# Performance work log

Measured on AMD Instinct MI355X. Metric: run time of the kernel, lower is better.

Reference implementation:

```python
import jax, jax.numpy as jnp
import numpy as np

H_DIM = 256
N_HEADS = 8
HEAD_DIM = H_DIM // N_HEADS
B, N = 2, 2048
LN_EPS = 1e-5


def setup_inputs() -> dict:
    key = jax.random.key(0)
    ks = jax.random.split(key, 20)
    s = 1.0 / np.sqrt(H_DIM)
    inp = {
        'hidden': jax.random.normal(ks[0], (B, N, H_DIM), jnp.float32),
        'adjacency': jax.random.uniform(ks[1], (B, N, N), jnp.float32),
        'positions': jax.random.uniform(ks[2], (B, N, 2), jnp.float32),
        # linear weights stored as (in, out): y = x @ W + b
        'wq': jax.random.normal(ks[3], (H_DIM, H_DIM), jnp.float32) * s,
        'bq': jnp.zeros((H_DIM,), jnp.float32),
        'wk': jax.random.normal(ks[4], (H_DIM, H_DIM), jnp.float32) * s,
        'bk': jnp.zeros((H_DIM,), jnp.float32),
        'wv': jax.random.normal(ks[5], (H_DIM, H_DIM), jnp.float32) * s,
        'bv': jnp.zeros((H_DIM,), jnp.float32),
        'wo': jax.random.normal(ks[6], (H_DIM, H_DIM), jnp.float32) * s,
        'bo': jnp.zeros((H_DIM,), jnp.float32),
        'g1': jnp.ones((H_DIM,), jnp.float32),
        'b1': jnp.zeros((H_DIM,), jnp.float32),
        'g2': jnp.ones((H_DIM,), jnp.float32),
        'b2': jnp.zeros((H_DIM,), jnp.float32),
        'w_ff1': jax.random.normal(ks[7], (H_DIM, 4 * H_DIM), jnp.float32) * s,
        'b_ff1': jnp.zeros((4 * H_DIM,), jnp.float32),
        'w_ff2': jax.random.normal(ks[8], (4 * H_DIM, H_DIM), jnp.float32) * (1.0 / np.sqrt(4 * H_DIM)),
        'b_ff2': jnp.zeros((H_DIM,), jnp.float32),
    }
    return inp


def _layernorm(x, g, b):
    mu = jnp.mean(x, axis=-1, keepdims=True)
    var = jnp.var(x, axis=-1, keepdims=True)
    return (x - mu) * jax.lax.rsqrt(var + LN_EPS) * g + b


def reference(hidden, adjacency, positions, wq, bq, wk, bk, wv, bv, wo, bo,
              g1, b1, g2, b2, w_ff1, b_ff1, w_ff2, b_ff2):
    b_, n_, _ = hidden.shape
    normalized = _layernorm(hidden, g1, b1)
    # project and split heads: [B, H, N, Dh]
    def heads(x):
        return x.reshape(b_, n_, N_HEADS, HEAD_DIM).transpose(0, 2, 1, 3)
    q = heads(normalized @ wq + bq)
    k = heads(normalized @ wk + bk)
    v = heads(normalized @ wv + bv)
    logits = jnp.einsum('bhnd,bhmd->bhnm', q, k) / np.sqrt(HEAD_DIM)
    cond = adjacency[:, None, :, :]  # mode == 'connectivity'
    logits = logits + (2.0 * cond - 1.0)
    weights = jax.nn.softmax(logits, axis=-1)
    weights = weights * (0.25 + 0.75 * cond)
    weights = weights / jnp.maximum(weights.sum(axis=-1, keepdims=True), 1e-6)
    attended = jnp.einsum('bhnm,bhmd->bhnd', weights, v)
    attended = attended.transpose(0, 2, 1, 3).reshape(b_, n_, H_DIM)
    hidden = hidden + attended @ wo + bo
    h2 = _layernorm(hidden, g2, b2)
    ff = jax.nn.gelu(h2 @ w_ff1 + b_ff1, approximate=False) @ w_ff2 + b_ff2
    return hidden + ff
```

## Files before the change

kernel.cpp:

```cpp
#include <hip/hip_runtime.h>
#include <math.h>

#define BB 2
#define NN 2048
#define HD 256
#define NH 8
#define DH 32
#define NTOK (BB*NN)
#define QKVLD 768
#define NSPLIT 2
#define KVPB (NN/NSPLIT)
#define NTILES (KVPB/64)

typedef _Float16 h8 __attribute__((ext_vector_type(8)));
typedef _Float16 h4 __attribute__((ext_vector_type(4)));
typedef float fx4 __attribute__((ext_vector_type(4)));

#define LOG2E 1.4426950408889634f
#define SQ_LOG2 0.25503486f
#define C1A (2.0f * LOG2E)
#define C0A (-(LOG2E + 6.0f))

__device__ __forceinline__ void ln_row(const float* __restrict__ x,
    const float* __restrict__ g, const float* __restrict__ bta,
    _Float16* __restrict__ yh, int row, int lane)
{
  const float* xr = x + (size_t)row * HD + lane * 4;
  float4 v = *(const float4*)xr;
  float s = v.x + v.y + v.z + v.w;
  #pragma unroll
  for (int off = 32; off > 0; off >>= 1) s += __shfl_xor(s, off);
  float mu = s * (1.0f / HD);
  float dx0 = v.x - mu, dx1 = v.y - mu, dx2 = v.z - mu, dx3 = v.w - mu;
  float ss = dx0*dx0 + dx1*dx1 + dx2*dx2 + dx3*dx3;
  #pragma unroll
  for (int off = 32; off > 0; off >>= 1) ss += __shfl_xor(ss, off);
  float rinv = rsqrtf(ss * (1.0f / HD) + 1e-5f);
  float4 gv = *(const float4*)(g   + lane * 4);
  float4 bv = *(const float4*)(bta + lane * 4);
  h4 hh;
  hh[0] = (_Float16)(dx0 * rinv * gv.x + bv.x);
  hh[1] = (_Float16)(dx1 * rinv * gv.y + bv.y);
  hh[2] = (_Float16)(dx2 * rinv * gv.z + bv.z);
  hh[3] = (_Float16)(dx3 * rinv * gv.w + bv.w);
  *(h4*)(yh + (size_t)row * HD + lane * 4) = hh;
}

__global__ __launch_bounds__(256) void ln_kernel(const float* __restrict__ x,
    const float* __restrict__ g, const float* __restrict__ bta,
    _Float16* __restrict__ yh)
{
  ln_row(x, g, bta, yh, blockIdx.x * 4 + (threadIdx.x >> 6), threadIdx.x & 63);
}

__device__ __forceinline__ void do_transpose(const float* __restrict__ W,
    _Float16* __restrict__ Wh, int Nw, int rowoff, int ldout, float scale,
    int bx, int by, float (*tile)[33])
{
  int k0 = by * 32, n0 = bx * 32;
  int c = threadIdx.x & 31, r = threadIdx.x >> 5;
  #pragma unroll
  for (int i = 0; i < 4; i++)
    tile[r + i * 8][c] = W[(size_t)(k0 + r + i * 8) * Nw + n0 + c];
  __syncthreads();
  #pragma unroll
  for (int i = 0; i < 4; i++) {
    int n = r + i * 8;
    Wh[(size_t)(rowoff + n0 + n) * ldout + k0 + c] = (_Float16)(tile[c][n] * scale);
  }
}

__global__ __launch_bounds__(256) void prep_kernel(
    const float* wq, const float* wk, const float* wv, const float* wo,
    const float* wf1, const float* wf2,
    const float* bq, const float* bk, const float* bv,
    const float* hidden, const float* g1, const float* b1,
    _Float16* WtQKVh, _Float16* WtOh, _Float16* WtF1h, _Float16* WtF2h,
    float* biasqkv, _Float16* norm1h)
{
  __shared__ float tile[32][33];
  int bid = blockIdx.x;
  if (bid < 64)        do_transpose(wq,  WtQKVh,  256,   0,  256, SQ_LOG2, bid & 7, bid >> 3, tile);
  else if (bid < 128)  do_transpose(wk,  WtQKVh,  256, 256,  256, 1.0f, (bid-64) & 7, (bid-64) >> 3, tile);
  else if (bid < 192)  do_transpose(wv,  WtQKVh,  256, 512,  256, 1.0f, (bid-128) & 7, (bid-128) >> 3, tile);
  else if (bid < 256)  do_transpose(wo,  WtOh,    256,   0,  256, 1.0f, (bid-192) & 7, (bid-192) >> 3, tile);
  else if (bid < 512)  do_transpose(wf1, WtF1h,  1024,   0,  256, 1.0f, (bid-256) & 31, (bid-256) >> 5, tile);
  else if (bid < 768)  do_transpose(wf2, WtF2h,   256,   0, 1024, 1.0f, (bid-512) & 7, (bid-512) >> 3, tile);
  else if (bid == 768) {
    #pragma unroll
    for (int j = 0; j < 3; j++) {
      int t = j * 256 + threadIdx.x;
      biasqkv[t] = (t < 256) ? bq[t] * SQ_LOG2 : (t < 512) ? bk[t - 256] : bv[t - 512];
    }
  } else {
    ln_row(hidden, g1, b1, norm1h, (bid - 769) * 4 + (threadIdx.x >> 6), threadIdx.x & 63);
  }
}

template<int KK, int NT, int NX, int ACT, int RES, int OM>
__global__ __launch_bounds__(256) void gemm16_kernel(
    const _Float16* __restrict__ Ah, const _Float16* __restrict__ Wh,
    const float* __restrict__ bias, const float* __restrict__ resid,
    float* __restrict__ Cf, _Float16* __restrict__ Ch,
    _Float16* __restrict__ vtb, int N)
{
  const int lin = blockIdx.x;
  const int qch = gridDim.x >> 3;
  const int wg = (lin & 7) * qch + (lin >> 3);
  const int bx = wg % NX, by = wg / NX;
  const int n0 = bx * (NT * 16);
  const int m0 = by * 64;
  const int t = threadIdx.x, w = t >> 6, l = t & 63;
  const int ml = l & 15, g = l >> 4;
  const int mrow = m0 + w * 16 + ml;

  const _Float16* aph = Ah + (size_t)mrow * KK + g * 8;
  const _Float16* whp[NT];
  #pragma unroll
  for (int nt = 0; nt < NT; nt++)
    whp[nt] = Wh + (size_t)(n0 + nt * 16 + ml) * KK + g * 8;

  fx4 acc[NT];
  #pragma unroll
  for (int nt = 0; nt < NT; nt++) acc[nt] = (fx4){0.f, 0.f, 0.f, 0.f};

  #pragma unroll 4
  for (int k0 = 0; k0 < KK; k0 += 32) {
    h8 ah = *(const h8*)(aph + k0);
    #pragma unroll
    for (int nt = 0; nt < NT; nt++) {
      h8 wh = *(const h8*)(whp[nt] + k0);
      acc[nt] = __builtin_amdgcn_mfma_f32_16x16x32_f16(ah, wh, acc[nt], 0, 0, 0);
    }
  }

  #pragma unroll
  for (int nt = 0; nt < NT; nt++) {
    int n = n0 + nt * 16 + ml;
    float bv = bias[n];
    #pragma unroll
    for (int i = 0; i < 4; i++) {
      int m = m0 + w * 16 + 4 * g + i;
      float vv = acc[nt][i] + bv;
      if (ACT == 1) vv = 0.5f * vv * (1.0f + erff(vv * 0.70710678118654752f));
      if (RES)      vv += resid[(size_t)m * N + n];
      if (OM == 0) {
        Cf[(size_t)m * N + n] = vv;
      } else if (OM == 1) {
        Ch[(size_t)m * N + n] = (_Float16)vv;
      } else {
        if (n < 512) Ch[(size_t)m * QKVLD + n] = (_Float16)vv;
        else {
          int dim = n - 512, kv = m & (NN - 1), bb = m >> 11;
          int kvp = (kv & ~31) | ((kv & 15) << 1) | ((kv >> 4) & 1);
          vtb[((size_t)(bb * HD + dim)) * NN + kvp] = (_Float16)vv;
        }
      }
    }
  }
}

__global__ __launch_bounds__(256) void wo_fused_kernel(
    const _Float16* __restrict__ Opart, const float* __restrict__ Spart,
    const _Float16* __restrict__ Wh, const float* __restrict__ bias,
    const float* __restrict__ resid, float* __restrict__ Cf)
{
  const int lin = blockIdx.x;
  const int qch = gridDim.x >> 3;
  const int wg = (lin & 7) * qch + (lin >> 3);
  const int bx = wg & 7, by = wg >> 3;
  const int n0 = bx * 32;
  const int m0 = by * 64;
  const int t = threadIdx.x, w = t >> 6, l = t & 63;
  const int ml = l & 15, g = l >> 4;
  const int mrow = m0 + w * 16 + ml;
  const int bb = mrow >> 11, qrow = mrow & (NN - 1);

  const _Float16* whp0 = Wh + (size_t)(n0 + ml) * HD + g * 8;
  const _Float16* whp1 = Wh + (size_t)(n0 + 16 + ml) * HD + g * 8;

  fx4 acc0 = {0.f, 0.f, 0.f, 0.f};
  fx4 acc1 = {0.f, 0.f, 0.f, 0.f};

  #pragma unroll
  for (int h = 0; h < NH; h++) {
    size_t p0 = ((size_t)((bb * 2 + 0) * NH + h)) * NN + qrow;
    size_t p1 = ((size_t)((bb * 2 + 1) * NH + h)) * NN + qrow;
    float s0 = Spart[p0], s1 = Spart[p1];
    float den = 1.0f / (s0 + s1);
    float w0 = s0 * den, w1 = s1 * den;
    h8 o0 = *(const h8*)(Opart + p0 * 32 + g * 8);
    h8 o1 = *(const h8*)(Opart + p1 * 32 + g * 8);
    h8 ah;
    #pragma unroll
    for (int j = 0; j < 8; j++)
      ah[j] = (_Float16)(w0 * (float)o0[j] + w1 * (float)o1[j]);
    h8 wh0 = *(const h8*)(whp0 + h * 32);
    h8 wh1 = *(const h8*)(whp1 + h * 32);
    acc0 = __builtin_amdgcn_mfma_f32_16x16x32_f16(ah, wh0, acc0, 0, 0, 0);
    acc1 = __builtin_amdgcn_mfma_f32_16x16x32_f16(ah, wh1, acc1, 0, 0, 0);
  }

  #pragma unroll
  for (int i = 0; i < 4; i++) {
    int m = m0 + w * 16 + 4 * g + i;
    int na = n0 + ml, nb = n0 + 16 + ml;
    Cf[(size_t)m * HD + na] = acc0[i] + bias[na] + resid[(size_t)m * HD + na];
    Cf[(size_t)m * HD + nb] = acc1[i] + bias[nb] + resid[(size_t)m * HD + nb];
  }
}

__global__ __launch_bounds__(256) void attn_mfma_kernel(
    const _Float16* __restrict__ qkv16, const _Float16* __restrict__ vtb,
    const float* __restrict__ adj,
    _Float16* __restrict__ Opart, float* __restrict__ Spart)
{
  __shared__ _Float16 Ksh[2][64][40];
  __shared__ _Float16 Vp[2][32][72];
  __shared__ _Float16 AdjL[2][64][68];

  const int z = blockIdx.z;
  const int b = z >> 1, half = z & 1;
  const int h = blockIdx.y;
  const int q0 = blockIdx.x * 64;
  const int t = threadIdx.x;
  const int w = t >> 6, l = t & 63;
  const int m = l & 15, g = l >> 4;
  const int kvbase = half * KVPB;

  const int qrow = q0 + w * 16 + m;
  h8 qh = *(const h8*)(qkv16 + ((size_t)(b * NN + qrow)) * QKVLD + h * DH + g * 8);

  fx4 ot0 = {0.f, 0.f, 0.f, 0.f};
  fx4 ot1 = {0.f, 0.f, 0.f, 0.f};
  float S4[4] = {0.f, 0.f, 0.f, 0.f};

  const int arow0 = t >> 4, acol = (t & 15) * 4;
  const float* adjbase = adj + ((size_t)(b * NN + q0)) * NN + kvbase;

  const int krow = t >> 2, kd0 = (t & 3) * 8;
  const int vdim = t >> 3, vkc = (t & 7) * 8;
  const _Float16* kbase = qkv16 + ((size_t)(b * NN + kvbase + krow)) * QKVLD + 256 + h * DH + kd0;
  const _Float16* vbase = vtb + ((size_t)(b * HD + h * DH + vdim)) * NN + kvbase + vkc;

  h8 kreg = *(const h8*)kbase;
  h8 vreg = *(const h8*)vbase;

  {
    float4 ar[4];
    #pragma unroll
    for (int j = 0; j < 4; j++)
      ar[j] = *(const float4*)(adjbase + (size_t)(j * 16 + arow0) * NN + acol);
    #pragma unroll
    for (int j = 0; j < 4; j++) {
      h4 hh;
      hh[0] = (_Float16)ar[j].x; hh[1] = (_Float16)ar[j].y;
      hh[2] = (_Float16)ar[j].z; hh[3] = (_Float16)ar[j].w;
      *(h4*)&AdjL[0][j * 16 + arow0][acol] = hh;
    }
  }
  *(h8*)&Ksh[0][krow][kd0] = kreg;
  *(h8*)&Vp[0][vdim][vkc]  = vreg;
  kreg = *(const h8*)(kbase + (size_t)64 * QKVLD);
  vreg = *(const h8*)(vbase + 64);
  __syncthreads();

  for (int tt = 0; tt < NTILES; ++tt) {
    const int cur = tt & 1;

    float4 ar[4];
    if (tt + 1 < NTILES) {
      #pragma unroll
      for (int j = 0; j < 4; j++)
        ar[j] = *(const float4*)(adjbase + (size_t)(j * 16 + arow0) * NN
                                 + (tt + 1) * 64 + acol);
    }

    h8 kh0 = *(const h8*)&Ksh[cur][     m][g * 8];
    h8 kh1 = *(const h8*)&Ksh[cur][16 + m][g * 8];
    h8 kh2 = *(const h8*)&Ksh[cur][32 + m][g * 8];
    h8 kh3 = *(const h8*)&Ksh[cur][48 + m][g * 8];
    fx4 z4 = {0.f, 0.f, 0.f, 0.f};
    fx4 st[4];
    st[0] = __builtin_amdgcn_mfma_f32_16x16x32_f16(kh0, qh, z4, 0, 0, 0);
    st[1] = __builtin_amdgcn_mfma_f32_16x16x32_f16(kh1, qh, z4, 0, 0, 0);
    st[2] = __builtin_amdgcn_mfma_f32_16x16x32_f16(kh2, qh, z4, 0, 0, 0);
    st[3] = __builtin_amdgcn_mfma_f32_16x16x32_f16(kh3, qh, z4, 0, 0, 0);

    float pv[16];
    #pragma unroll
    for (int p = 0; p < 4; p++) {
      h4 ah4 = *(const h4*)&AdjL[cur][w * 16 + m][p * 16 + g * 4];
      float ps = 0.f;
      #pragma unroll
      for (int i = 0; i < 4; i++) {
        float a = (float)ah4[i];
        float e = __builtin_amdgcn_exp2f(st[p][i] + C1A * a + C0A);
        float pp = (0.25f + 0.75f * a) * e;
        pv[p * 4 + i] = pp;
        ps += pp;
      }
      S4[p] += ps;
    }
    h8 ph0, ph1;
    #pragma unroll
    for (int q2 = 0; q2 < 4; q2++) {
      ph0[2*q2]     = (_Float16)pv[q2];
      ph0[2*q2 + 1] = (_Float16)pv[4 + q2];
      ph1[2*q2]     = (_Float16)pv[8 + q2];
      ph1[2*q2 + 1] = (_Float16)pv[12 + q2];
    }

    h8 v00 = *(const h8*)&Vp[cur][m][g * 8];
    h8 v01 = *(const h8*)&Vp[cur][m][32 + g * 8];
    h8 v10 = *(const h8*)&Vp[cur][16 + m][g * 8];
    h8 v11 = *(const h8*)&Vp[cur][16 + m][32 + g * 8];
    ot0 = __builtin_amdgcn_mfma_f32_16x16x32_f16(v00, ph0, ot0, 0, 0, 0);
    ot0 = __builtin_amdgcn_mfma_f32_16x16x32_f16(v01, ph1, ot0, 0, 0, 0);
    ot1 = __builtin_amdgcn_mfma_f32_16x16x32_f16(v10, ph0, ot1, 0, 0, 0);
    ot1 = __builtin_amdgcn_mfma_f32_16x16x32_f16(v11, ph1, ot1, 0, 0, 0);

    if (tt + 1 < NTILES) {
      #pragma unroll
      for (int j = 0; j < 4; j++) {
        h4 hh;
        hh[0] = (_Float16)ar[j].x; hh[1] = (_Float16)ar[j].y;
        hh[2] = (_Float16)ar[j].z; hh[3] = (_Float16)ar[j].w;
        *(h4*)&AdjL[cur ^ 1][j * 16 + arow0][acol] = hh;
      }
      *(h8*)&Ksh[cur ^ 1][krow][kd0] = kreg;
      *(h8*)&Vp[cur ^ 1][vdim][vkc]  = vreg;
      if (tt + 2 < NTILES) {
        kreg = *(const h8*)(kbase + (size_t)((tt + 2) * 64) * QKVLD);
        vreg = *(const h8*)(vbase + (tt + 2) * 64);
      }
    }
    __syncthreads();
  }

  float S = (S4[0] + S4[1]) + (S4[2] + S4[3]);
  S += __shfl_xor(S, 16);
  S += __shfl_xor(S, 32);

  float is = 1.0f / S;
  size_t prow = ((size_t)(z * NH + h)) * NN + qrow;
  _Float16* po = Opart + prow * 32;
  h4 o0h, o1h;
  #pragma unroll
  for (int j = 0; j < 4; j++) {
    o0h[j] = (_Float16)(ot0[j] * is);
    o1h[j] = (_Float16)(ot1[j] * is);
  }
  *(h4*)(po + 4 * g)      = o0h;
  *(h4*)(po + 16 + 4 * g) = o1h;
  if (g == 0) Spart[prow] = S;
}

extern "C" void kernel_launch(void* const* d_in, const int* in_sizes, int n_in,
                              void* d_out, int out_size, void* d_ws, size_t ws_size,
                              hipStream_t stream)
{
  const float* hidden    = (const float*)d_in[0];
  const float* adjacency = (const float*)d_in[1];
  const float* wq  = (const float*)d_in[3];
  const float* bq  = (const float*)d_in[4];
  const float* wk  = (const float*)d_in[5];
  const float* bk  = (const float*)d_in[6];
  const float* wv  = (const float*)d_in[7];
  const float* bv  = (const float*)d_in[8];
  const float* wo  = (const float*)d_in[9];
  const float* bo  = (const float*)d_in[10];
  const float* g1  = (const float*)d_in[11];
  const float* b1  = (const float*)d_in[12];
  const float* g2  = (const float*)d_in[13];
  const float* b2  = (const float*)d_in[14];
  const float* wf1 = (const float*)d_in[15];
  const float* bf1 = (const float*)d_in[16];
  const float* wf2 = (const float*)d_in[17];
  const float* bf2 = (const float*)d_in[18];
  float* out = (float*)d_out;

  char* base = (char*)d_ws;
  const size_t MB = 1024 * 1024;
  _Float16* norm1h = (_Float16*)(base);
  _Float16* qkv16  = (_Float16*)(base + 2*MB);
  _Float16* vtb    = (_Float16*)(base + 8*MB);
  float*    hid2   = (float*)(base + 12*MB);
  _Float16* Opart = (_Float16*)(base + 16*MB);
  _Float16* ffah  = (_Float16*)(base + 16*MB);
  float* Spart = (float*)(base + 25*MB);
  _Float16* wtb = (_Float16*)(base + 26*MB);
  _Float16* WtQKVh = wtb; wtb += 768 * 256;
  _Float16* WtOh   = wtb; wtb += 256 * 256;
  _Float16* WtF1h  = wtb; wtb += 1024 * 256;
  _Float16* WtF2h  = wtb; wtb += 256 * 1024;
  float* biasqkv = (float*)(base + 28*MB);

  prep_kernel<<<1793, 256, 0, stream>>>(wq, wk, wv, wo, wf1, wf2, bq, bk, bv,
      hidden, g1, b1, WtQKVh, WtOh, WtF1h, WtF2h, biasqkv, norm1h);

  gemm16_kernel<256, 2, 24, 0, 0, 2><<<1536, 256, 0, stream>>>(
      norm1h, WtQKVh, biasqkv, nullptr, nullptr, qkv16, vtb, QKVLD);

  attn_mfma_kernel<<<dim3(NN / 64, NH, BB * NSPLIT), 256, 0, stream>>>(
      qkv16, vtb, adjacency, Opart, Spart);

  wo_fused_kernel<<<512, 256, 0, stream>>>(
      Opart, Spart, WtOh, bo, hidden, hid2);

  ln_kernel<<<NTOK / 4, 256, 0, stream>>>(hid2, g2, b2, norm1h);

  gemm16_kernel<256, 2, 32, 1, 0, 1><<<2048, 256, 0, stream>>>(
      norm1h, WtF1h, bf1, nullptr, nullptr, ffah, nullptr, 1024);

  gemm16_kernel<1024, 1, 16, 0, 1, 0><<<1024, 256, 0, stream>>>(
      ffah, WtF2h, bf2, hid2, out, nullptr, nullptr, 256);
}
```

Measured before the change: 131.6 us.

## Share adjacency tile across two heads per attention block; retile GEMMs

The attention kernel now processes two heads per 512-thread block, so each adjacency tile loaded from global memory and converted to fp16 is reused by both heads instead of being re-read per head. This halves adjacency traffic, the dominant memory stream (B*N*N floats read once per head). K/V shared buffers are duplicated per head, raising LDS use per block. Separately, the three GEMM launches change template tiling parameters, doubling work per block and halving grid sizes.

```diff
diff --git a/kernel.cpp b/kernel.cpp
--- a/kernel.cpp
+++ b/kernel.cpp
@@ -210,57 +210,61 @@
   }
 }
 
-__global__ __launch_bounds__(256) void attn_mfma_kernel(
+__global__ __launch_bounds__(512) void attn_mfma_kernel(
     const _Float16* __restrict__ qkv16, const _Float16* __restrict__ vtb,
     const float* __restrict__ adj,
     _Float16* __restrict__ Opart, float* __restrict__ Spart)
 {
-  __shared__ _Float16 Ksh[2][64][40];
-  __shared__ _Float16 Vp[2][32][72];
+  __shared__ _Float16 Ksh[2][2][64][40];
+  __shared__ _Float16 Vp[2][2][32][72];
   __shared__ _Float16 AdjL[2][64][68];
 
   const int z = blockIdx.z;
   const int b = z >> 1, half = z & 1;
-  const int h = blockIdx.y;
+  const int hg = blockIdx.y;
   const int q0 = blockIdx.x * 64;
   const int t = threadIdx.x;
-  const int w = t >> 6, l = t & 63;
+  const int hh_ = t >> 8;
+  const int head = hg * 2 + hh_;
+  const int tl = t & 255;
+  const int w = tl >> 6, l = t & 63;
   const int m = l & 15, g = l >> 4;
   const int kvbase = half * KVPB;
 
   const int qrow = q0 + w * 16 + m;
-  h8 qh = *(const h8*)(qkv16 + ((size_t)(b * NN + qrow)) * QKVLD + h * DH + g * 8);
+  h8 qh = *(const h8*)(qkv16 + ((size_t)(b * NN + qrow)) * QKVLD + head * DH + g * 8);
 
   fx4 ot0 = {0.f, 0.f, 0.f, 0.f};
   fx4 ot1 = {0.f, 0.f, 0.f, 0.f};
   float S4[4] = {0.f, 0.f, 0.f, 0.f};
 
-  const int arow0 = t >> 4, acol = (t & 15) * 4;
+  const int arow0 = t >> 4;
+  const int acol = (t & 15) * 4;
   const float* adjbase = adj + ((size_t)(b * NN + q0)) * NN + kvbase;
 
-  const int krow = t >> 2, kd0 = (t & 3) * 8;
-  const int vdim = t >> 3, vkc = (t & 7) * 8;
-  const _Float16* kbase = qkv16 + ((size_t)(b * NN + kvbase + krow)) * QKVLD + 256 + h * DH + kd0;
-  const _Float16* vbase = vtb + ((size_t)(b * HD + h * DH + vdim)) * NN + kvbase + vkc;
+  const int krow = tl >> 2, kd0 = (tl & 3) * 8;
+  const int vdim = tl >> 3, vkc = (tl & 7) * 8;
+  const _Float16* kbase = qkv16 + ((size_t)(b * NN + kvbase + krow)) * QKVLD + 256 + head * DH + kd0;
+  const _Float16* vbase = vtb + ((size_t)(b * HD + head * DH + vdim)) * NN + kvbase + vkc;
 
   h8 kreg = *(const h8*)kbase;
   h8 vreg = *(const h8*)vbase;
 
   {
-    float4 ar[4];
-    #pragma unroll
-    for (int j = 0; j < 4; j++)
-      ar[j] = *(const float4*)(adjbase + (size_t)(j * 16 + arow0) * NN + acol);
-    #pragma unroll
-    for (int j = 0; j < 4; j++) {
+    float4 ar[2];
+    #pragma unroll
+    for (int j = 0; j < 2; j++)
+      ar[j] = *(const float4*)(adjbase + (size_t)(j * 32 + arow0) * NN + acol);
+    #pragma unroll
+    for (int j = 0; j < 2; j++) {
       h4 hh;
       hh[0] = (_Float16)ar[j].x; hh[1] = (_Float16)ar[j].y;
       hh[2] = (_Float16)ar[j].z; hh[3] = (_Float16)ar[j].w;
-      *(h4*)&AdjL[0][j * 16 + arow0][acol] = hh;
-    }
-  }
-  *(h8*)&Ksh[0][krow][kd0] = kreg;
-  *(h8*)&Vp[0][vdim][vkc]  = vreg;
+      *(h4*)&AdjL[0][j * 32 + arow0][acol] = hh;
+    }
+  }
+  *(h8*)&Ksh[hh_][0][krow][kd0] = kreg;
+  *(h8*)&Vp[hh_][0][vdim][vkc]  = vreg;
   kreg = *(const h8*)(kbase + (size_t)64 * QKVLD);
   vreg = *(const h8*)(vbase + 64);
   __syncthreads();
@@ -268,18 +272,18 @@
   for (int tt = 0; tt < NTILES; ++tt) {
     const int cur = tt & 1;
 
-    float4 ar[4];
+    float4 ar[2];
     if (tt + 1 < NTILES) {
       #pragma unroll
-      for (int j = 0; j < 4; j++)
-        ar[j] = *(const float4*)(adjbase + (size_t)(j * 16 + arow0) * NN
+      for (int j = 0; j < 2; j++)
+        ar[j] = *(const float4*)(adjbase + (size_t)(j * 32 + arow0) * NN
                                  + (tt + 1) * 64 + acol);
     }
 
-    h8 kh0 = *(const h8*)&Ksh[cur][     m][g * 8];
-    h8 kh1 = *(const h8*)&Ksh[cur][16 + m][g * 8];
-    h8 kh2 = *(const h8*)&Ksh[cur][32 + m][g * 8];
-    h8 kh3 = *(const h8*)&Ksh[cur][48 + m][g * 8];
+    h8 kh0 = *(const h8*)&Ksh[hh_][cur][     m][g * 8];
+    h8 kh1 = *(const h8*)&Ksh[hh_][cur][16 + m][g * 8];
+    h8 kh2 = *(const h8*)&Ksh[hh_][cur][32 + m][g * 8];
+    h8 kh3 = *(const h8*)&Ksh[hh_][cur][48 + m][g * 8];
     fx4 z4 = {0.f, 0.f, 0.f, 0.f};
     fx4 st[4];
     st[0] = __builtin_amdgcn_mfma_f32_16x16x32_f16(kh0, qh, z4, 0, 0, 0);
@@ -311,10 +315,10 @@
       ph1[2*q2 + 1] = (_Float16)pv[12 + q2];
     }
 
-    h8 v00 = *(const h8*)&Vp[cur][m][g * 8];
-    h8 v01 = *(const h8*)&Vp[cur][m][32 + g * 8];
-    h8 v10 = *(const h8*)&Vp[cur][16 + m][g * 8];
-    h8 v11 = *(const h8*)&Vp[cur][16 + m][32 + g * 8];
+    h8 v00 = *(const h8*)&Vp[hh_][cur][m][g * 8];
+    h8 v01 = *(const h8*)&Vp[hh_][cur][m][32 + g * 8];
+    h8 v10 = *(const h8*)&Vp[hh_][cur][16 + m][g * 8];
+    h8 v11 = *(const h8*)&Vp[hh_][cur][16 + m][32 + g * 8];
     ot0 = __builtin_amdgcn_mfma_f32_16x16x32_f16(v00, ph0, ot0, 0, 0, 0);
     ot0 = __builtin_amdgcn_mfma_f32_16x16x32_f16(v01, ph1, ot0, 0, 0, 0);
     ot1 = __builtin_amdgcn_mfma_f32_16x16x32_f16(v10, ph0, ot1, 0, 0, 0);
@@ -322,14 +326,14 @@
 
     if (tt + 1 < NTILES) {
       #pragma unroll
-      for (int j = 0; j < 4; j++) {
+      for (int j = 0; j < 2; j++) {
         h4 hh;
         hh[0] = (_Float16)ar[j].x; hh[1] = (_Float16)ar[j].y;
         hh[2] = (_Float16)ar[j].z; hh[3] = (_Float16)ar[j].w;
-        *(h4*)&AdjL[cur ^ 1][j * 16 + arow0][acol] = hh;
+        *(h4*)&AdjL[cur ^ 1][j * 32 + arow0][acol] = hh;
       }
-      *(h8*)&Ksh[cur ^ 1][krow][kd0] = kreg;
-      *(h8*)&Vp[cur ^ 1][vdim][vkc]  = vreg;
+      *(h8*)&Ksh[hh_][cur ^ 1][krow][kd0] = kreg;
+      *(h8*)&Vp[hh_][cur ^ 1][vdim][vkc]  = vreg;
       if (tt + 2 < NTILES) {
         kreg = *(const h8*)(kbase + (size_t)((tt + 2) * 64) * QKVLD);
         vreg = *(const h8*)(vbase + (tt + 2) * 64);
@@ -343,7 +347,7 @@
   S += __shfl_xor(S, 32);
 
   float is = 1.0f / S;
-  size_t prow = ((size_t)(z * NH + h)) * NN + qrow;
+  size_t prow = ((size_t)(z * NH + head)) * NN + qrow;
   _Float16* po = Opart + prow * 32;
   h4 o0h, o1h;
   #pragma unroll
@@ -399,10 +403,10 @@
   prep_kernel<<<1793, 256, 0, stream>>>(wq, wk, wv, wo, wf1, wf2, bq, bk, bv,
       hidden, g1, b1, WtQKVh, WtOh, WtF1h, WtF2h, biasqkv, norm1h);
 
-  gemm16_kernel<256, 2, 24, 0, 0, 2><<<1536, 256, 0, stream>>>(
+  gemm16_kernel<256, 4, 12, 0, 0, 2><<<768, 256, 0, stream>>>(
       norm1h, WtQKVh, biasqkv, nullptr, nullptr, qkv16, vtb, QKVLD);
 
-  attn_mfma_kernel<<<dim3(NN / 64, NH, BB * NSPLIT), 256, 0, stream>>>(
+  attn_mfma_kernel<<<dim3(NN / 64, NH / 2, BB * NSPLIT), 512, 0, stream>>>(
       qkv16, vtb, adjacency, Opart, Spart);
 
   wo_fused_kernel<<<512, 256, 0, stream>>>(
@@ -410,9 +414,9 @@
 
   ln_kernel<<<NTOK / 4, 256, 0, stream>>>(hid2, g2, b2, norm1h);
 
-  gemm16_kernel<256, 2, 32, 1, 0, 1><<<2048, 256, 0, stream>>>(
+  gemm16_kernel<256, 4, 16, 1, 0, 1><<<1024, 256, 0, stream>>>(
       norm1h, WtF1h, bf1, nullptr, nullptr, ffah, nullptr, 1024);
 
-  gemm16_kernel<1024, 1, 16, 0, 1, 0><<<1024, 256, 0, stream>>>(
+  gemm16_kernel<1024, 2, 8, 0, 1, 0><<<512, 256, 0, stream>>>(
       ffah, WtF2h, bf2, hid2, out, nullptr, nullptr, 256);
 }
```

Result: faster. 117.2 us (-10.9%).
